# Optimization experiments

Hardware: AMD Instinct MI355X
Metric: run time of the kernel (lower is better)

Reference implementation:

```python
import jax, jax.numpy as jnp
import numpy as np

B, S, D, E, K = 4, 4096, 2048, 64, 8

def setup_inputs() -> dict:
    key = jax.random.key(0)
    k1, k2 = jax.random.split(key, 2)
    x = jax.random.normal(k1, (B, S, D), dtype=jnp.float32)
    # centroid projection params (Dense(features=n_experts))
    W = jax.random.normal(k2, (D, E), dtype=jnp.float32) / np.sqrt(D).astype(np.float32)
    b = jnp.zeros((E,), dtype=jnp.float32)
    return {"x": x, "W": W, "b": b, "k": K}

def reference(x, W, b, k):
    # dense gating projection + sigmoid -> per-token expert scores [B,S,E]
    scores = jax.nn.sigmoid(jnp.einsum('bsd,de->bse', x, W) + b)
    # per-token top-k expert selection (vectorized form of apply_along_axis(top))
    g_i, idx = jax.lax.top_k(scores, k)          # [B,S,k]
    g = g_i / jnp.sum(g_i, axis=-1, keepdims=True)  # renormalize top-k gates
    return g, idx, scores
```

## Files before the change

### kernel.cpp

```cpp
#include <hip/hip_runtime.h>
#include <math.h>

#define NTOK   16384
#define DDIM   2048
#define NE     64
#define TOPK   8

#define THREADS 512
#define NWAVE   8
#define TOKPB   64
#define BK      128
#define KSLICE  (BK / NWAVE)

#define SBIDX(t,e) ((t)*67 + ((e) ^ ((t) >> 3)))

__global__ __launch_bounds__(THREADS) void gate_kernel(
    const float* __restrict__ x, const float* __restrict__ W,
    const float* __restrict__ b, float* __restrict__ out)
{
    __shared__ float smem[16384];

    const int tid  = threadIdx.x;
    const int wave = tid >> 6;
    const int lane = tid & 63;
    const int tg   = lane >> 3;
    const int eg   = lane & 7;
    const int tok0 = blockIdx.x * TOKPB;

    float acc[8][8];
#pragma unroll
    for (int i = 0; i < 8; ++i)
#pragma unroll
        for (int j = 0; j < 8; ++j) acc[i][j] = 0.f;

    const int kw0 = wave * KSLICE;
    const int st_t  = tid >> 3;
    const int st_k4 = tid & 7;

    for (int c = 0; c < DDIM / BK; ++c) {
        const int kc = c * BK;
        __syncthreads();
#pragma unroll
        for (int jj = 0; jj < 4; ++jj) {
            const int k4 = st_k4 + jj * 8;
            const float4 v = *(const float4*)&x[(size_t)(tok0 + st_t) * DDIM + kc + k4 * 4];
            smem[(k4 * 4 + 0) * 64 + st_t] = v.x;
            smem[(k4 * 4 + 1) * 64 + st_t] = v.y;
            smem[(k4 * 4 + 2) * 64 + st_t] = v.z;
            smem[(k4 * 4 + 3) * 64 + st_t] = v.w;
        }
        {
            const float4* Wg = (const float4*)&W[(size_t)kc * NE];
#pragma unroll
            for (int jj = 0; jj < 4; ++jj) {
                const int slot = tid + jj * THREADS;
                *(float4*)&smem[8192 + slot * 4] = Wg[slot];
            }
        }
        __syncthreads();
#pragma unroll
        for (int kk = 0; kk < KSLICE; ++kk) {
            const int k = kw0 + kk;
            const float4 xa = *(const float4*)&smem[k * 64 + tg * 8];
            const float4 xb = *(const float4*)&smem[k * 64 + tg * 8 + 4];
            const float4 wa = *(const float4*)&smem[8192 + k * 64 + eg * 8];
            const float4 wb = *(const float4*)&smem[8192 + k * 64 + eg * 8 + 4];
            const float xs[8] = {xa.x, xa.y, xa.z, xa.w, xb.x, xb.y, xb.z, xb.w};
            const float ws[8] = {wa.x, wa.y, wa.z, wa.w, wb.x, wb.y, wb.z, wb.w};
#pragma unroll
            for (int i = 0; i < 8; ++i)
#pragma unroll
                for (int j = 0; j < 8; ++j)
                    acc[i][j] = fmaf(xs[i], ws[j], acc[i][j]);
        }
    }

    __syncthreads();
    for (int s = tid; s < 64 * 67; s += THREADS) smem[s] = 0.f;
    __syncthreads();
#pragma unroll
    for (int i = 0; i < 8; ++i)
#pragma unroll
        for (int j = 0; j < 8; ++j) {
            const int t = tg * 8 + i;
            const int e = eg * 8 + j;
            atomicAdd(&smem[SBIDX(t, e)], acc[i][j]);
        }
    __syncthreads();

    float* out_g   = out;
    float* out_idx = out + (size_t)NTOK * TOPK;
    float* out_s   = out + (size_t)NTOK * TOPK * 2;

#pragma unroll
    for (int r = 0; r < 8; ++r) {
        const int flat = r * THREADS + tid;
        const int t = flat >> 6;
        const int e = flat & 63;
        const float z = smem[SBIDX(t, e)] + b[e];
        const float s = 1.f / (1.f + expf(-z));
        out_s[(size_t)tok0 * NE + flat] = s;
        smem[SBIDX(t, e)] = s;
    }
    __syncthreads();

    if (tid < TOKPB) {
        const int t = tid;
        float gv[TOPK];
        int   gi[TOPK];
        float sum = 0.f;
#pragma unroll
        for (int j = 0; j < TOPK; ++j) {
            float best = -1.f;
            int bi = 0;
            for (int e = 0; e < NE; ++e) {
                const float v = smem[SBIDX(t, e)];
                if (v > best) { best = v; bi = e; }
            }
            gv[j] = best; gi[j] = bi; sum += best;
            smem[SBIDX(t, bi)] = -2.f;
        }
        const float inv = 1.f / sum;
#pragma unroll
        for (int j = 0; j < TOPK; ++j) {
            out_g[(size_t)(tok0 + t) * TOPK + j]   = gv[j] * inv;
            out_idx[(size_t)(tok0 + t) * TOPK + j] = (float)gi[j];
        }
    }
}

extern "C" void kernel_launch(void* const* d_in, const int* in_sizes, int n_in,
                              void* d_out, int out_size, void* d_ws, size_t ws_size,
                              hipStream_t stream) {
    const float* x = (const float*)d_in[0];
    const float* W = (const float*)d_in[1];
    const float* b = (const float*)d_in[2];
    float* out = (float*)d_out;
    gate_kernel<<<NTOK / TOKPB, THREADS, 0, stream>>>(x, W, b, out);
}
```

Before: 274.5 us.

## Prefetch next x/W chunk into registers and swizzle transposed x smem layout

Loads for the next K-chunk of x and W are issued into registers right after the current chunk is written to shared memory, so global latency overlaps the FMA loop. The transposed x tile in shared memory gets an XOR swizzle by k-group to spread the scalar scatter stores across banks. This adds 32 registers of prefetch state on top of the 64 accumulators, which may pressure occupancy.

Result: slower. 323.0 us (+17.7%).

```diff
diff --git a/kernel.cpp b/kernel.cpp
--- a/kernel.cpp
+++ b/kernel.cpp
@@ -10,7 +10,10 @@
 #define NWAVE   8
 #define TOKPB   64
 #define BK      128
-#define KSLICE  (BK / NWAVE)
+#define NCHUNK (DDIM / BK)
+#define KSLICE (BK / NWAVE)
+
+#define XSWZ(k)  ((((k) >> 2) & 7) * 8)
 
 #define SBIDX(t,e) ((t)*67 + ((e) ^ ((t) >> 3)))
 
@@ -36,33 +39,49 @@
     const int kw0 = wave * KSLICE;
     const int st_t  = tid >> 3;
     const int st_k4 = tid & 7;
+    const float* xrow = &x[(size_t)(tok0 + st_t) * DDIM];
 
-    for (int c = 0; c < DDIM / BK; ++c) {
-        const int kc = c * BK;
+    float4 rx[4], rw[4];
+#pragma unroll
+    for (int jj = 0; jj < 4; ++jj)
+        rx[jj] = *(const float4*)&xrow[(st_k4 + jj * 8) * 4];
+#pragma unroll
+    for (int jj = 0; jj < 4; ++jj)
+        rw[jj] = ((const float4*)W)[tid + jj * THREADS];
+
+    for (int c = 0; c < NCHUNK; ++c) {
         __syncthreads();
 #pragma unroll
         for (int jj = 0; jj < 4; ++jj) {
-            const int k4 = st_k4 + jj * 8;
-            const float4 v = *(const float4*)&x[(size_t)(tok0 + st_t) * DDIM + kc + k4 * 4];
-            smem[(k4 * 4 + 0) * 64 + st_t] = v.x;
-            smem[(k4 * 4 + 1) * 64 + st_t] = v.y;
-            smem[(k4 * 4 + 2) * 64 + st_t] = v.z;
-            smem[(k4 * 4 + 3) * 64 + st_t] = v.w;
+            const int k4   = st_k4 + jj * 8;
+            const int base = st_t ^ XSWZ(k4 * 4);
+            const float4 v = rx[jj];
+            smem[(k4 * 4 + 0) * 64 + base] = v.x;
+            smem[(k4 * 4 + 1) * 64 + base] = v.y;
+            smem[(k4 * 4 + 2) * 64 + base] = v.z;
+            smem[(k4 * 4 + 3) * 64 + base] = v.w;
         }
-        {
-            const float4* Wg = (const float4*)&W[(size_t)kc * NE];
 #pragma unroll
-            for (int jj = 0; jj < 4; ++jj) {
-                const int slot = tid + jj * THREADS;
-                *(float4*)&smem[8192 + slot * 4] = Wg[slot];
-            }
+        for (int jj = 0; jj < 4; ++jj)
+            *(float4*)&smem[8192 + (tid + jj * THREADS) * 4] = rw[jj];
+
+        if (c + 1 < NCHUNK) {
+            const int kc = (c + 1) * BK;
+#pragma unroll
+            for (int jj = 0; jj < 4; ++jj)
+                rx[jj] = *(const float4*)&xrow[kc + (st_k4 + jj * 8) * 4];
+#pragma unroll
+            for (int jj = 0; jj < 4; ++jj)
+                rw[jj] = *(const float4*)&W[(size_t)kc * NE + (tid + jj * THREADS) * 4];
         }
         __syncthreads();
+
 #pragma unroll
         for (int kk = 0; kk < KSLICE; ++kk) {
-            const int k = kw0 + kk;
-            const float4 xa = *(const float4*)&smem[k * 64 + tg * 8];
-            const float4 xb = *(const float4*)&smem[k * 64 + tg * 8 + 4];
+            const int k    = kw0 + kk;
+            const int xoff = k * 64 + ((tg * 8) ^ XSWZ(k));
+            const float4 xa = *(const float4*)&smem[xoff];
+            const float4 xb = *(const float4*)&smem[xoff + 4];
             const float4 wa = *(const float4*)&smem[8192 + k * 64 + eg * 8];
             const float4 wb = *(const float4*)&smem[8192 + k * 64 + eg * 8 + 4];
             const float xs[8] = {xa.x, xa.y, xa.z, xa.w, xb.x, xb.y, xb.z, xb.w};
```

## Double-buffer global-to-LDS loads with direct async copies and smaller token tiles

Applied to the files above, without the earlier changes.

Replaces register-staged transposed copies of x and W into shared memory with direct global_load_lds async copies into a double buffer, so the next chunk loads while the current one is computed. Halves tokens per block to 32 and the K chunk to 64, which shrinks the accumulator to 4x8 and targets two blocks per CU through launch bounds. The trade-off is more blocks, each re-reading W, and more per-block reduction and top-k overhead relative to the work done.

Measured after the change: 262.2 us. 1.05x faster.

```diff
diff --git a/kernel.cpp b/kernel.cpp
--- a/kernel.cpp
+++ b/kernel.cpp
@@ -1,5 +1,6 @@
 #include <hip/hip_runtime.h>
 #include <math.h>
+#include <stdint.h>
 
 #define NTOK   16384
 #define DDIM   2048
@@ -8,17 +9,29 @@
 
 #define THREADS 512
 #define NWAVE   8
-#define TOKPB   64
-#define BK      128
+#define TOKPB   32
+#define BK      64
+#define NCHUNK  (DDIM / BK)
 #define KSLICE  (BK / NWAVE)
 
-#define SBIDX(t,e) ((t)*67 + ((e) ^ ((t) >> 3)))
+#define XSLOTS   ((BK / 4) * TOKPB)
+#define WSLOTS   (BK * (NE / 4))
+#define BUFSLOTS (XSLOTS + WSLOTS)
 
-__global__ __launch_bounds__(THREADS) void gate_kernel(
+#define SBIDX(t,e) ((t)*67 + ((e) ^ ((t) & 7)))
+
+__device__ __forceinline__ void gl_lds16(const void* g, void* l) {
+    __builtin_amdgcn_global_load_lds(
+        (const __attribute__((address_space(1))) void*)(uintptr_t)g,
+        (__attribute__((address_space(3))) void*)(uintptr_t)l,
+        16, 0, 0);
+}
+
+__global__ __launch_bounds__(THREADS, 2) void gate_kernel(
     const float* __restrict__ x, const float* __restrict__ W,
     const float* __restrict__ b, float* __restrict__ out)
 {
-    __shared__ float smem[16384];
+    __shared__ float4 smem[2 * BUFSLOTS];
 
     const int tid  = threadIdx.x;
     const int wave = tid >> 6;
@@ -27,65 +40,68 @@
     const int eg   = lane & 7;
     const int tok0 = blockIdx.x * TOKPB;
 
-    float acc[8][8];
+    const int st_k4 = tid >> 5;
+    const int st_sg = lane & 31;
+    const int st_t  = 4 * (st_sg & 7) + (st_sg >> 3);
+    const float* gx  = x + (size_t)(tok0 + st_t) * DDIM + st_k4 * 4;
+    const float* gw0 = W + (size_t)(wave * 128 + lane) * 4;
+    const float* gw1 = gw0 + 64 * 4;
+
+    float acc[4][8];
 #pragma unroll
-    for (int i = 0; i < 8; ++i)
+    for (int i = 0; i < 4; ++i)
 #pragma unroll
         for (int j = 0; j < 8; ++j) acc[i][j] = 0.f;
 
-    const int kw0 = wave * KSLICE;
-    const int st_t  = tid >> 3;
-    const int st_k4 = tid & 7;
+    auto stage = [&](int c) {
+        float4* B = &smem[(c & 1) * BUFSLOTS];
+        const int kc = c * BK;
+        gl_lds16(gx + kc,             &B[wave * 64]);
+        gl_lds16(gw0 + (size_t)kc * NE, &B[XSLOTS + wave * 128]);
+        gl_lds16(gw1 + (size_t)kc * NE, &B[XSLOTS + wave * 128 + 64]);
+    };
 
-    for (int c = 0; c < DDIM / BK; ++c) {
-        const int kc = c * BK;
-        __syncthreads();
+    stage(0);
+    __syncthreads();
+
+    for (int c = 0; c < NCHUNK; ++c) {
+        if (c + 1 < NCHUNK) stage(c + 1);
+        const float4* BX = &smem[(c & 1) * BUFSLOTS];
+        const float4* BW = BX + XSLOTS;
 #pragma unroll
-        for (int jj = 0; jj < 4; ++jj) {
-            const int k4 = st_k4 + jj * 8;
-            const float4 v = *(const float4*)&x[(size_t)(tok0 + st_t) * DDIM + kc + k4 * 4];
-            smem[(k4 * 4 + 0) * 64 + st_t] = v.x;
-            smem[(k4 * 4 + 1) * 64 + st_t] = v.y;
-            smem[(k4 * 4 + 2) * 64 + st_t] = v.z;
-            smem[(k4 * 4 + 3) * 64 + st_t] = v.w;
-        }
-        {
-            const float4* Wg = (const float4*)&W[(size_t)kc * NE];
+        for (int g = 0; g < 2; ++g) {
+            const int k4 = wave * 2 + g;
+            float4 xv[4];
 #pragma unroll
-            for (int jj = 0; jj < 4; ++jj) {
-                const int slot = tid + jj * THREADS;
-                *(float4*)&smem[8192 + slot * 4] = Wg[slot];
+            for (int i = 0; i < 4; ++i)
+                xv[i] = BX[k4 * 32 + tg + 8 * i];
+#pragma unroll
+            for (int kk = 0; kk < 4; ++kk) {
+                const int k = k4 * 4 + kk;
+                const float4 wa = BW[k * 16 + eg * 2];
+                const float4 wb = BW[k * 16 + eg * 2 + 1];
+                const float ws[8] = {wa.x, wa.y, wa.z, wa.w,
+                                     wb.x, wb.y, wb.z, wb.w};
+#pragma unroll
+                for (int i = 0; i < 4; ++i) {
+                    const float xs = ((const float*)&xv[i])[kk];
+#pragma unroll
+                    for (int j = 0; j < 8; ++j)
+                        acc[i][j] = fmaf(xs, ws[j], acc[i][j]);
+                }
             }
         }
         __syncthreads();
-#pragma unroll
-        for (int kk = 0; kk < KSLICE; ++kk) {
-            const int k = kw0 + kk;
-            const float4 xa = *(const float4*)&smem[k * 64 + tg * 8];
-            const float4 xb = *(const float4*)&smem[k * 64 + tg * 8 + 4];
-            const float4 wa = *(const float4*)&smem[8192 + k * 64 + eg * 8];
-            const float4 wb = *(const float4*)&smem[8192 + k * 64 + eg * 8 + 4];
-            const float xs[8] = {xa.x, xa.y, xa.z, xa.w, xb.x, xb.y, xb.z, xb.w};
-            const float ws[8] = {wa.x, wa.y, wa.z, wa.w, wb.x, wb.y, wb.z, wb.w};
-#pragma unroll
-            for (int i = 0; i < 8; ++i)
-#pragma unroll
-                for (int j = 0; j < 8; ++j)
-                    acc[i][j] = fmaf(xs[i], ws[j], acc[i][j]);
-        }
     }
 
-    __syncthreads();
-    for (int s = tid; s < 64 * 67; s += THREADS) smem[s] = 0.f;
+    float* sb = (float*)smem;
+    for (int s = tid; s < TOKPB * 67; s += THREADS) sb[s] = 0.f;
     __syncthreads();
 #pragma unroll
-    for (int i = 0; i < 8; ++i)
+    for (int i = 0; i < 4; ++i)
 #pragma unroll
-        for (int j = 0; j < 8; ++j) {
-            const int t = tg * 8 + i;
-            const int e = eg * 8 + j;
-            atomicAdd(&smem[SBIDX(t, e)], acc[i][j]);
-        }
+        for (int j = 0; j < 8; ++j)
+            atomicAdd(&sb[SBIDX(tg * 4 + i, eg * 8 + j)], acc[i][j]);
     __syncthreads();
 
     float* out_g   = out;
@@ -93,14 +109,14 @@
     float* out_s   = out + (size_t)NTOK * TOPK * 2;
 
 #pragma unroll
-    for (int r = 0; r < 8; ++r) {
+    for (int r = 0; r < (TOKPB * NE) / THREADS; ++r) {
         const int flat = r * THREADS + tid;
         const int t = flat >> 6;
         const int e = flat & 63;
-        const float z = smem[SBIDX(t, e)] + b[e];
+        const float z = sb[SBIDX(t, e)] + b[e];
         const float s = 1.f / (1.f + expf(-z));
         out_s[(size_t)tok0 * NE + flat] = s;
-        smem[SBIDX(t, e)] = s;
+        sb[SBIDX(t, e)] = s;
     }
     __syncthreads();
 
@@ -114,11 +130,11 @@
             float best = -1.f;
             int bi = 0;
             for (int e = 0; e < NE; ++e) {
-                const float v = smem[SBIDX(t, e)];
+                const float v = sb[SBIDX(t, e)];
                 if (v > best) { best = v; bi = e; }
             }
             gv[j] = best; gi[j] = bi; sum += best;
-            smem[SBIDX(t, bi)] = -2.f;
+            sb[SBIDX(t, bi)] = -2.f;
         }
         const float inv = 1.f / sum;
 #pragma unroll
```

## Replace LDS-tiled GEMM with per-token register accumulation and scalar W loads

Applied to the files above, without the earlier changes.

Each thread now owns one token and accumulates all 64 expert dot products in registers over a k-slice assigned to its wave, with 16 waves splitting the reduction dimension. W is read through the constant address space with wave-uniform indices so it can use scalar loads, and x is read directly from global memory, removing per-chunk LDS staging and barriers. Partial sums are combined via shared-memory atomics as before. Risks include uncoalesced strided x row reads, high register pressure from 64 accumulators, and scalar-load throughput limits.

After: 328.3 us. 1.2x slower.

```diff
diff --git a/kernel.cpp b/kernel.cpp
--- a/kernel.cpp
+++ b/kernel.cpp
@@ -1,91 +1,58 @@
 #include <hip/hip_runtime.h>
 #include <math.h>
+#include <stdint.h>
 
 #define NTOK   16384
 #define DDIM   2048
 #define NE     64
 #define TOPK   8
 
-#define THREADS 512
-#define NWAVE   8
+#define THREADS 1024
+#define NWAVE   16
 #define TOKPB   64
-#define BK      128
-#define KSLICE  (BK / NWAVE)
+#define KPW     (DDIM / NWAVE)
 
-#define SBIDX(t,e) ((t)*67 + ((e) ^ ((t) >> 3)))
+#define SBIDX(t,e) ((t)*67 + ((e) ^ ((t) & 7)))
 
-__global__ __launch_bounds__(THREADS) void gate_kernel(
+typedef const __attribute__((address_space(4))) float* cfptr;
+
+__global__ __launch_bounds__(THREADS, 1) void gate_kernel(
     const float* __restrict__ x, const float* __restrict__ W,
     const float* __restrict__ b, float* __restrict__ out)
 {
-    __shared__ float smem[16384];
+    __shared__ float sb[TOKPB * 67];
 
     const int tid  = threadIdx.x;
-    const int wave = tid >> 6;
-    const int lane = tid & 63;
-    const int tg   = lane >> 3;
-    const int eg   = lane & 7;
+    const int t    = tid & 63;
+    const int wv   = __builtin_amdgcn_readfirstlane(tid >> 6);
     const int tok0 = blockIdx.x * TOKPB;
 
-    float acc[8][8];
+    cfptr Wc = (cfptr)(uintptr_t)W;
+
+    float acc[NE];
 #pragma unroll
-    for (int i = 0; i < 8; ++i)
+    for (int e = 0; e < NE; ++e) acc[e] = 0.f;
+
+    const float4* xrow = (const float4*)(x + (size_t)(tok0 + t) * DDIM + wv * KPW);
+
+    for (int k4 = 0; k4 < KPW / 4; ++k4) {
+        const float4 xv = xrow[k4];
+        const float xs[4] = {xv.x, xv.y, xv.z, xv.w};
 #pragma unroll
-        for (int j = 0; j < 8; ++j) acc[i][j] = 0.f;
-
-    const int kw0 = wave * KSLICE;
-    const int st_t  = tid >> 3;
-    const int st_k4 = tid & 7;
-
-    for (int c = 0; c < DDIM / BK; ++c) {
-        const int kc = c * BK;
-        __syncthreads();
+        for (int kk = 0; kk < 4; ++kk) {
+            const int k = wv * KPW + k4 * 4 + kk;
+            cfptr wr = Wc + (size_t)k * NE;
 #pragma unroll
-        for (int jj = 0; jj < 4; ++jj) {
-            const int k4 = st_k4 + jj * 8;
-            const float4 v = *(const float4*)&x[(size_t)(tok0 + st_t) * DDIM + kc + k4 * 4];
-            smem[(k4 * 4 + 0) * 64 + st_t] = v.x;
-            smem[(k4 * 4 + 1) * 64 + st_t] = v.y;
-            smem[(k4 * 4 + 2) * 64 + st_t] = v.z;
-            smem[(k4 * 4 + 3) * 64 + st_t] = v.w;
-        }
-        {
-            const float4* Wg = (const float4*)&W[(size_t)kc * NE];
-#pragma unroll
-            for (int jj = 0; jj < 4; ++jj) {
-                const int slot = tid + jj * THREADS;
-                *(float4*)&smem[8192 + slot * 4] = Wg[slot];
-            }
-        }
-        __syncthreads();
-#pragma unroll
-        for (int kk = 0; kk < KSLICE; ++kk) {
-            const int k = kw0 + kk;
-            const float4 xa = *(const float4*)&smem[k * 64 + tg * 8];
-            const float4 xb = *(const float4*)&smem[k * 64 + tg * 8 + 4];
-            const float4 wa = *(const float4*)&smem[8192 + k * 64 + eg * 8];
-            const float4 wb = *(const float4*)&smem[8192 + k * 64 + eg * 8 + 4];
-            const float xs[8] = {xa.x, xa.y, xa.z, xa.w, xb.x, xb.y, xb.z, xb.w};
-            const float ws[8] = {wa.x, wa.y, wa.z, wa.w, wb.x, wb.y, wb.z, wb.w};
-#pragma unroll
-            for (int i = 0; i < 8; ++i)
-#pragma unroll
-                for (int j = 0; j < 8; ++j)
-                    acc[i][j] = fmaf(xs[i], ws[j], acc[i][j]);
+            for (int e = 0; e < NE; ++e)
+                acc[e] = fmaf(xs[kk], wr[e], acc[e]);
         }
     }
 
-    __syncthreads();
-    for (int s = tid; s < 64 * 67; s += THREADS) smem[s] = 0.f;
+    for (int s = tid; s < TOKPB * 67; s += THREADS) sb[s] = 0.f;
     __syncthreads();
 #pragma unroll
-    for (int i = 0; i < 8; ++i)
-#pragma unroll
-        for (int j = 0; j < 8; ++j) {
-            const int t = tg * 8 + i;
-            const int e = eg * 8 + j;
-            atomicAdd(&smem[SBIDX(t, e)], acc[i][j]);
-        }
+    for (int e = 0; e < NE; ++e)
+        atomicAdd(&sb[SBIDX(t, e)], acc[e]);
     __syncthreads();
 
     float* out_g   = out;
@@ -93,19 +60,18 @@
     float* out_s   = out + (size_t)NTOK * TOPK * 2;
 
 #pragma unroll
-    for (int r = 0; r < 8; ++r) {
+    for (int r = 0; r < (TOKPB * NE) / THREADS; ++r) {
         const int flat = r * THREADS + tid;
-        const int t = flat >> 6;
-        const int e = flat & 63;
-        const float z = smem[SBIDX(t, e)] + b[e];
+        const int tt = flat >> 6;
+        const int e  = flat & 63;
+        const float z = sb[SBIDX(tt, e)] + b[e];
         const float s = 1.f / (1.f + expf(-z));
         out_s[(size_t)tok0 * NE + flat] = s;
-        smem[SBIDX(t, e)] = s;
+        sb[SBIDX(tt, e)] = s;
     }
     __syncthreads();
 
     if (tid < TOKPB) {
-        const int t = tid;
         float gv[TOPK];
         int   gi[TOPK];
         float sum = 0.f;
@@ -114,17 +80,17 @@
             float best = -1.f;
             int bi = 0;
             for (int e = 0; e < NE; ++e) {
-                const float v = smem[SBIDX(t, e)];
+                const float v = sb[SBIDX(tid, e)];
                 if (v > best) { best = v; bi = e; }
             }
             gv[j] = best; gi[j] = bi; sum += best;
-            smem[SBIDX(t, bi)] = -2.f;
+            sb[SBIDX(tid, bi)] = -2.f;
         }
         const float inv = 1.f / sum;
 #pragma unroll
         for (int j = 0; j < TOPK; ++j) {
-            out_g[(size_t)(tok0 + t) * TOPK + j]   = gv[j] * inv;
-            out_idx[(size_t)(tok0 + t) * TOPK + j] = (float)gi[j];
+            out_g[(size_t)(tok0 + tid) * TOPK + j]   = gv[j] * inv;
+            out_idx[(size_t)(tok0 + tid) * TOPK + j] = (float)gi[j];
         }
     }
 }
```
